# Kernel optimization log

Measured on AMD Instinct MI355X. Metric: run time of the kernel, lower is better.

## Reference

```python
import jax, jax.numpy as jnp
import numpy as np

EPS = 1.1920929e-07  # torch fp32 finfo eps used by F.rms_norm default

def rms_norm(x):
    return x * jax.lax.rsqrt(jnp.mean(jnp.square(x), axis=-1, keepdims=True) + EPS)

def setup_inputs() -> dict:
    key = jax.random.key(0)
    kx, kfc, kpr, krt = jax.random.split(key, 4)
    B, T, C, F = 4, 2048, 2048, 8192
    s = (3.0 ** 0.5) * C ** -0.5  # init scale used in init_weights
    x = jax.random.normal(kx, (B, T, C), dtype=jnp.float32)
    w_fc = jax.random.normal(kfc, (F, C), dtype=jnp.float32) * s
    w_proj = jax.random.normal(kpr, (C, F), dtype=jnp.float32) * (s * 0.1)
    w_router = jax.random.normal(krt, (1, C), dtype=jnp.float32) * 0.01  # router init std=0.01
    return {"x": x, "w_fc": w_fc, "w_proj": w_proj, "w_router": w_router}

def reference(x, w_fc, w_proj, w_router):
    # Router: (B,T,C) @ (C,1) -> (B,T) logits; STE mask (~0 or ~1 floats)
    logits = jnp.einsum('btc,oc->bto', x, w_router)[..., 0]  # (B,T)
    prob = jax.nn.sigmoid(logits)
    hard = (prob > 0.5).astype(x.dtype)
    mask_i = hard + prob - jax.lax.stop_gradient(prob)  # straight-through
    mask_bool = mask_i > 0.5  # (B,T)

    # Gated MLP (mixture-of-depth). The torch code gathers selected tokens,
    # runs the MLP on the compacted set, scatters into zeros, and multiplies
    # by mask_i. Mathematically identical dense form (honoring the mask):
    h = jnp.einsum('btc,fc->btf', rms_norm(x), w_fc)
    h = jnp.square(jax.nn.relu(h))  # relu(x)^2 activation
    mlp_out = jnp.einsum('btf,cf->btc', h, w_proj)
    gated = jnp.where(mask_bool[..., None], mlp_out * mask_i[..., None], 0.0)
    return x + gated
```

## Files before the change

### kernel.cpp

```cpp
#include <hip/hip_runtime.h>
#include <type_traits>
#include <utility>
#include <stdint.h>
#include <stddef.h>

#define TOKENS 8192
#define CDIM 2048
#define FDIM 8192
#define EPSV 1.1920929e-07f

typedef __attribute__((ext_vector_type(8))) short short8;
typedef __attribute__((ext_vector_type(8))) __bf16 bf16x8;
typedef __attribute__((ext_vector_type(4))) float floatx4;

template <typename V, typename = void> struct CanMfma : std::false_type {};
template <typename V>
struct CanMfma<V, std::void_t<decltype(__builtin_amdgcn_mfma_f32_16x16x32_bf16(
    std::declval<V>(), std::declval<V>(), std::declval<floatx4>(), 0, 0, 0))>>
    : std::true_type {};
using frag_t = std::conditional_t<CanMfma<short8>::value, short8, bf16x8>;

__device__ __forceinline__ floatx4 mfma_bf16(frag_t a, frag_t b, floatx4 c) {
    return __builtin_amdgcn_mfma_f32_16x16x32_bf16(a, b, c, 0, 0, 0);
}

__device__ __forceinline__ unsigned short f2bf(float f) {
    unsigned int u = __float_as_uint(f);
    u += 0x7fffu + ((u >> 16) & 1u);
    return (unsigned short)(u >> 16);
}

__global__ void zero_kernel(int* p) { if (threadIdx.x == 0) *p = 0; }

__global__ __launch_bounds__(256) void cvt2_kernel(
    const float* __restrict__ s1, unsigned short* __restrict__ d1, int n1,
    const float* __restrict__ s2, unsigned short* __restrict__ d2, int n2)
{
    int i = blockIdx.x * 256 + threadIdx.x;
    const float4* s; ushort4* d;
    if (i < n1) { s = (const float4*)s1; d = (ushort4*)d1; }
    else if (i < n1 + n2) { s = (const float4*)s2; d = (ushort4*)d2; i -= n1; }
    else return;
    float4 v = s[i];
    ushort4 o;
    o.x = f2bf(v.x); o.y = f2bf(v.y); o.z = f2bf(v.z); o.w = f2bf(v.w);
    d[i] = o;
}

__global__ __launch_bounds__(256) void router_kernel(
    const float* __restrict__ x, const float* __restrict__ wr,
    float* __restrict__ out, unsigned short* __restrict__ Xn,
    int* __restrict__ idx, float* __restrict__ mv, int* __restrict__ cnt)
{
    const int token = blockIdx.x;
    const int tid = threadIdx.x;
    const float4* xr = (const float4*)(x + (size_t)token * CDIM);
    const float4* w4 = (const float4*)wr;
    float4 a0 = xr[tid];
    float4 a1 = xr[tid + 256];
    float4 b0 = w4[tid];
    float4 b1 = w4[tid + 256];
    float ss = a0.x*a0.x + a0.y*a0.y + a0.z*a0.z + a0.w*a0.w
             + a1.x*a1.x + a1.y*a1.y + a1.z*a1.z + a1.w*a1.w;
    float dt = a0.x*b0.x + a0.y*b0.y + a0.z*b0.z + a0.w*b0.w
             + a1.x*b1.x + a1.y*b1.y + a1.z*b1.z + a1.w*b1.w;
    #pragma unroll
    for (int off = 32; off > 0; off >>= 1) {
        ss += __shfl_down(ss, off);
        dt += __shfl_down(dt, off);
    }
    __shared__ float red_ss[4], red_dt[4];
    __shared__ float s_rms;
    __shared__ int s_pos;
    const int wave = tid >> 6;
    if ((tid & 63) == 0) { red_ss[wave] = ss; red_dt[wave] = dt; }
    __syncthreads();
    if (tid == 0) {
        float S = red_ss[0] + red_ss[1] + red_ss[2] + red_ss[3];
        float D = red_dt[0] + red_dt[1] + red_dt[2] + red_dt[3];
        float prob = 1.0f / (1.0f + expf(-D));
        s_rms = 1.0f / sqrtf(S * (1.0f / (float)CDIM) + EPSV);
        int pos = -1;
        if (prob > 0.5f) {
            pos = atomicAdd(cnt, 1);
            idx[pos] = token;
            mv[pos] = (1.0f + prob) - prob;
        }
        s_pos = pos;
    }
    __syncthreads();
    float4* op = (float4*)(out + (size_t)token * CDIM);
    op[tid] = a0;
    op[tid + 256] = a1;
    const float rms = s_rms;
    const int pos = s_pos;
    if (pos >= 0) {
        ushort4* xp = (ushort4*)(Xn + (size_t)pos * CDIM);
        ushort4 o;
        o.x = f2bf(a0.x * rms); o.y = f2bf(a0.y * rms); o.z = f2bf(a0.z * rms); o.w = f2bf(a0.w * rms);
        xp[tid] = o;
        o.x = f2bf(a1.x * rms); o.y = f2bf(a1.y * rms); o.z = f2bf(a1.z * rms); o.w = f2bf(a1.w * rms);
        xp[tid + 256] = o;
    }
}

template <int K, int MODE, int LDO, int KSPLIT>
__global__ __launch_bounds__(256) void gemm_bt(
    const unsigned short* __restrict__ A,
    const unsigned short* __restrict__ B,
    unsigned short* __restrict__ Hout,
    float* __restrict__ out,
    const int* __restrict__ idx,
    const float* __restrict__ mv,
    const int* __restrict__ cntp)
{
    const int cnt = *cntp;
    const int bid = blockIdx.y * 64 + blockIdx.x;
    const int s = bid >> 6;
    const int w = bid & 63;
    const int mi = (s & 7) * 8 + (w & 7);
    const int ni = (s >> 3) * 8 + (w >> 3);
    const int m0 = mi * 128;
    if (m0 >= cnt) return;
    const int n0 = ni * 128;
    const int k0 = (int)blockIdx.z * (K / KSPLIT);

    __shared__ alignas(16) unsigned short lA[128 * 64];
    __shared__ alignas(16) unsigned short lB[128 * 64];

    const int tid = threadIdx.x;
    const int wave = tid >> 6;
    const int lane = tid & 63;
    const int wm = (wave >> 1) * 64;
    const int wn = (wave & 1) * 64;
    const int quad = lane >> 4;
    const int l16 = lane & 15;

    const int srow = lane >> 3;
    const int schunk = (lane & 7) ^ srow;

    const unsigned short* ap[4];
    const unsigned short* bp[4];
    #pragma unroll
    for (int p = 0; p < 4; ++p) {
        const int r = p * 32 + wave * 8 + srow;
        ap[p] = A + (size_t)(m0 + r) * K + k0 + schunk * 8;
        bp[p] = B + (size_t)(n0 + r) * K + k0 + schunk * 8;
    }

    floatx4 acc[4][4] = {};

    for (int kt = 0; kt < K / (64 * KSPLIT); ++kt) {
        #pragma unroll
        for (int p = 0; p < 4; ++p) {
            __builtin_amdgcn_global_load_lds(
                (__attribute__((address_space(1))) void*)ap[p],
                (__attribute__((address_space(3))) void*)&lA[(p * 32 + wave * 8) * 64],
                16, 0, 0);
            __builtin_amdgcn_global_load_lds(
                (__attribute__((address_space(1))) void*)bp[p],
                (__attribute__((address_space(3))) void*)&lB[(p * 32 + wave * 8) * 64],
                16, 0, 0);
            ap[p] += 64;
            bp[p] += 64;
        }
        __syncthreads();
        #pragma unroll
        for (int st = 0; st < 2; ++st) {
            frag_t af[4], bfv[4];
            #pragma unroll
            for (int t = 0; t < 4; ++t) {
                const int ra = wm + t * 16 + l16;
                const int ca = ((st * 4 + quad) ^ (ra & 7)) * 8;
                af[t] = *(const frag_t*)&lA[ra * 64 + ca];
                const int rb = wn + t * 16 + l16;
                const int cb = ((st * 4 + quad) ^ (rb & 7)) * 8;
                bfv[t] = *(const frag_t*)&lB[rb * 64 + cb];
            }
            #pragma unroll
            for (int tm = 0; tm < 4; ++tm)
                #pragma unroll
                for (int tn = 0; tn < 4; ++tn)
                    acc[tm][tn] = mfma_bf16(af[tm], bfv[tn], acc[tm][tn]);
        }
        __syncthreads();
    }

    if (MODE == 1) {
        #pragma unroll
        for (int tm = 0; tm < 4; ++tm) {
            const int gm = m0 + wm + tm * 16 + quad * 4;
            #pragma unroll
            for (int tn = 0; tn < 4; ++tn) {
                const int gn = n0 + wn + tn * 16 + l16;
                #pragma unroll
                for (int v = 0; v < 4; ++v) {
                    float h = fmaxf(acc[tm][tn][v], 0.0f);
                    Hout[(size_t)(gm + v) * LDO + gn] = f2bf(h * h);
                }
            }
        }
    } else {
        #pragma unroll
        for (int tm = 0; tm < 4; ++tm) {
            const int gmb = m0 + wm + tm * 16 + quad * 4;
            #pragma unroll
            for (int v = 0; v < 4; ++v) {
                const int gm = gmb + v;
                if (gm < cnt) {
                    const int token = idx[gm];
                    const float scale = mv[gm];
                    #pragma unroll
                    for (int tn = 0; tn < 4; ++tn) {
                        const int gn = n0 + wn + tn * 16 + l16;
                        atomicAdd(&out[(size_t)token * LDO + gn], scale * acc[tm][tn][v]);
                    }
                }
            }
        }
    }
}

extern "C" void kernel_launch(void* const* d_in, const int* in_sizes, int n_in,
                              void* d_out, int out_size, void* d_ws, size_t ws_size,
                              hipStream_t stream)
{
    const float* x   = (const float*)d_in[0];
    const float* wfc = (const float*)d_in[1];
    const float* wpr = (const float*)d_in[2];
    const float* wrt = (const float*)d_in[3];
    float* out = (float*)d_out;

    char* ws = (char*)d_ws;
    int*   cnt = (int*)ws;
    int*   idx = (int*)(ws + 256);
    float* mv  = (float*)(ws + 256 + 32768);
    unsigned short* Xn  = (unsigned short*)(ws + 65792);
    unsigned short* Wfc = (unsigned short*)(ws + 65792 + 33554432ULL);
    unsigned short* Wpr = (unsigned short*)(ws + 65792 + 67108864ULL);
    unsigned short* H   = (unsigned short*)(ws + 65792 + 100663296ULL);

    const int n4 = FDIM * CDIM / 4;
    zero_kernel<<<1, 64, 0, stream>>>(cnt);
    cvt2_kernel<<<(2 * n4 + 255) / 256, 256, 0, stream>>>(wfc, Wfc, n4, wpr, Wpr, n4);
    router_kernel<<<TOKENS, 256, 0, stream>>>(x, wrt, out, Xn, idx, mv, cnt);
    gemm_bt<CDIM, 1, FDIM, 1><<<dim3(64, FDIM / 128), 256, 0, stream>>>(
        Xn, Wfc, H, nullptr, nullptr, nullptr, cnt);
    gemm_bt<FDIM, 2, CDIM, 2><<<dim3(64, CDIM / 128, 2), 256, 0, stream>>>(
        H, Wpr, nullptr, out, idx, mv, cnt);
}
```

Measured before the change: 704.5 us.

## Double-buffer LDS tiles in GEMM and remap block-to-tile swizzle

Adds a second LDS buffer for the A and B tiles. The next K-slice is issued with global_load_lds before computing on the current one, so global-to-LDS transfer overlaps MFMA work and one barrier per iteration is removed. It also changes the block-to-(m,n) tile mapping within each 64-block group to a 4x... sub-grouping, aiming for better L2 reuse across concurrently running blocks. LDS use doubles to 64KB per block, which may reduce occupancy. Correctness relies on the asynchronous LDS writes being complete at the trailing barrier.

```diff
diff --git a/kernel.cpp b/kernel.cpp
--- a/kernel.cpp
+++ b/kernel.cpp
@@ -118,15 +118,17 @@
     const int bid = blockIdx.y * 64 + blockIdx.x;
     const int s = bid >> 6;
     const int w = bid & 63;
-    const int mi = (s & 7) * 8 + (w & 7);
-    const int ni = (s >> 3) * 8 + (w >> 3);
+    const int r = w & 7;
+    const int t = w >> 3;
+    const int mi = (s & 7) * 8 + (r >> 2) * 4 + (t & 3);
+    const int ni = (s >> 3) * 8 + (r & 3) * 2 + (t >> 2);
     const int m0 = mi * 128;
     if (m0 >= cnt) return;
     const int n0 = ni * 128;
     const int k0 = (int)blockIdx.z * (K / KSPLIT);
 
-    __shared__ alignas(16) unsigned short lA[128 * 64];
-    __shared__ alignas(16) unsigned short lB[128 * 64];
+    __shared__ alignas(16) unsigned short lA[2][128 * 64];
+    __shared__ alignas(16) unsigned short lB[2][128 * 64];
 
     const int tid = threadIdx.x;
     const int wave = tid >> 6;
@@ -143,39 +145,47 @@
     const unsigned short* bp[4];
     #pragma unroll
     for (int p = 0; p < 4; ++p) {
-        const int r = p * 32 + wave * 8 + srow;
-        ap[p] = A + (size_t)(m0 + r) * K + k0 + schunk * 8;
-        bp[p] = B + (size_t)(n0 + r) * K + k0 + schunk * 8;
-    }
-
-    floatx4 acc[4][4] = {};
-
-    for (int kt = 0; kt < K / (64 * KSPLIT); ++kt) {
+        const int rr = p * 32 + wave * 8 + srow;
+        ap[p] = A + (size_t)(m0 + rr) * K + k0 + schunk * 8;
+        bp[p] = B + (size_t)(n0 + rr) * K + k0 + schunk * 8;
+    }
+
+    auto stage = [&](int buf) {
         #pragma unroll
         for (int p = 0; p < 4; ++p) {
             __builtin_amdgcn_global_load_lds(
                 (__attribute__((address_space(1))) void*)ap[p],
-                (__attribute__((address_space(3))) void*)&lA[(p * 32 + wave * 8) * 64],
+                (__attribute__((address_space(3))) void*)&lA[buf][(p * 32 + wave * 8) * 64],
                 16, 0, 0);
             __builtin_amdgcn_global_load_lds(
                 (__attribute__((address_space(1))) void*)bp[p],
-                (__attribute__((address_space(3))) void*)&lB[(p * 32 + wave * 8) * 64],
+                (__attribute__((address_space(3))) void*)&lB[buf][(p * 32 + wave * 8) * 64],
                 16, 0, 0);
             ap[p] += 64;
             bp[p] += 64;
         }
-        __syncthreads();
+    };
+
+    floatx4 acc[4][4] = {};
+
+    const int NT = K / (64 * KSPLIT);
+    int cur = 0;
+    stage(0);
+    __syncthreads();
+
+    for (int kt = 0; kt < NT; ++kt) {
+        if (kt + 1 < NT) stage(cur ^ 1);
         #pragma unroll
         for (int st = 0; st < 2; ++st) {
             frag_t af[4], bfv[4];
             #pragma unroll
-            for (int t = 0; t < 4; ++t) {
-                const int ra = wm + t * 16 + l16;
+            for (int tt = 0; tt < 4; ++tt) {
+                const int ra = wm + tt * 16 + l16;
                 const int ca = ((st * 4 + quad) ^ (ra & 7)) * 8;
-                af[t] = *(const frag_t*)&lA[ra * 64 + ca];
-                const int rb = wn + t * 16 + l16;
+                af[tt] = *(const frag_t*)&lA[cur][ra * 64 + ca];
+                const int rb = wn + tt * 16 + l16;
                 const int cb = ((st * 4 + quad) ^ (rb & 7)) * 8;
-                bfv[t] = *(const frag_t*)&lB[rb * 64 + cb];
+                bfv[tt] = *(const frag_t*)&lB[cur][rb * 64 + cb];
             }
             #pragma unroll
             for (int tm = 0; tm < 4; ++tm)
@@ -184,6 +194,7 @@
                     acc[tm][tn] = mfma_bf16(af[tm], bfv[tn], acc[tm][tn]);
         }
         __syncthreads();
+        cur ^= 1;
     }
 
     if (MODE == 1) {
```

Result: slower. 754.5 us (+7.1%).

## Use 256x256 GEMM tiles with 512 threads and 4-stage LDS pipeline

Applied to the files above, without the earlier changes.

Both bf16 GEMMs now use 256x256 output tiles computed by 8 waves, each wave holding an 8x4 block of MFMA accumulators. The K step drops to 32, and a 4-buffer, 128KB dynamic LDS ring is filled through global_load_lds with three stages in flight. Explicit vmcnt waits, barriers and setprio are added around the MFMA block. The aim is more data reuse per tile and loads that overlap compute, at the cost of higher register pressure, a single block per CU, and fewer blocks for the second GEMM.

```diff
diff --git a/kernel.cpp b/kernel.cpp
--- a/kernel.cpp
+++ b/kernel.cpp
@@ -105,7 +105,7 @@
 }
 
 template <int K, int MODE, int LDO, int KSPLIT>
-__global__ __launch_bounds__(256) void gemm_bt(
+__global__ __launch_bounds__(512, 2) void gemm_bt(
     const unsigned short* __restrict__ A,
     const unsigned short* __restrict__ B,
     unsigned short* __restrict__ Hout,
@@ -115,95 +115,121 @@
     const int* __restrict__ cntp)
 {
     const int cnt = *cntp;
-    const int bid = blockIdx.y * 64 + blockIdx.x;
+    const int bid = blockIdx.y * 32 + blockIdx.x;
     const int s = bid >> 6;
     const int w = bid & 63;
-    const int mi = (s & 7) * 8 + (w & 7);
-    const int ni = (s >> 3) * 8 + (w >> 3);
-    const int m0 = mi * 128;
+    const int mi = (s & 3) * 8 + (w & 7);
+    const int ni = (s >> 2) * 8 + (w >> 3);
+    const int m0 = mi * 256;
     if (m0 >= cnt) return;
-    const int n0 = ni * 128;
+    const int n0 = ni * 256;
     const int k0 = (int)blockIdx.z * (K / KSPLIT);
 
-    __shared__ alignas(16) unsigned short lA[128 * 64];
-    __shared__ alignas(16) unsigned short lB[128 * 64];
+    extern __shared__ unsigned short lds[];
 
     const int tid = threadIdx.x;
     const int wave = tid >> 6;
     const int lane = tid & 63;
-    const int wm = (wave >> 1) * 64;
-    const int wn = (wave & 1) * 64;
+    const int wm = (wave >> 2) * 128;
+    const int wn = (wave & 3) * 64;
     const int quad = lane >> 4;
     const int l16 = lane & 15;
 
-    const int srow = lane >> 3;
-    const int schunk = (lane & 7) ^ srow;
-
-    const unsigned short* ap[4];
-    const unsigned short* bp[4];
+    const int srow = 2 * (tid >> 3) + ((tid >> 2) & 1);
+    const int sq   = (tid & 3) ^ ((tid >> 3) & 3);
+
+    const unsigned short* ap[2];
+    const unsigned short* bp[2];
     #pragma unroll
-    for (int p = 0; p < 4; ++p) {
-        const int r = p * 32 + wave * 8 + srow;
-        ap[p] = A + (size_t)(m0 + r) * K + k0 + schunk * 8;
-        bp[p] = B + (size_t)(n0 + r) * K + k0 + schunk * 8;
-    }
-
-    floatx4 acc[4][4] = {};
-
-    for (int kt = 0; kt < K / (64 * KSPLIT); ++kt) {
-        #pragma unroll
-        for (int p = 0; p < 4; ++p) {
+    for (int p = 0; p < 2; ++p) {
+        const int r = p * 128 + srow;
+        ap[p] = A + (size_t)(m0 + r) * K + k0 + sq * 8;
+        bp[p] = B + (size_t)(n0 + r) * K + k0 + sq * 8;
+    }
+
+    auto stage = [&](int v) {
+        unsigned short* base = &lds[(v & 3) * 16384];
+        #pragma unroll
+        for (int p = 0; p < 2; ++p) {
             __builtin_amdgcn_global_load_lds(
                 (__attribute__((address_space(1))) void*)ap[p],
-                (__attribute__((address_space(3))) void*)&lA[(p * 32 + wave * 8) * 64],
+                (__attribute__((address_space(3))) void*)&base[(p * 512 + wave * 64) * 8],
                 16, 0, 0);
+            ap[p] += 32;
+        }
+        #pragma unroll
+        for (int p = 0; p < 2; ++p) {
             __builtin_amdgcn_global_load_lds(
                 (__attribute__((address_space(1))) void*)bp[p],
-                (__attribute__((address_space(3))) void*)&lB[(p * 32 + wave * 8) * 64],
+                (__attribute__((address_space(3))) void*)&base[8192 + (p * 512 + wave * 64) * 8],
                 16, 0, 0);
-            ap[p] += 64;
-            bp[p] += 64;
-        }
-        __syncthreads();
-        #pragma unroll
-        for (int st = 0; st < 2; ++st) {
-            frag_t af[4], bfv[4];
+            bp[p] += 32;
+        }
+    };
+
+    floatx4 acc[8][4] = {};
+
+    const int NT = K / (32 * KSPLIT);
+    stage(0); stage(1); stage(2);
+
+    for (int u = 0; u < NT; ++u) {
+        const int rem = NT - 1 - u;
+        if (rem >= 3) {
+            stage(u + 3);
+            asm volatile("s_waitcnt vmcnt(12)" ::: "memory");
+        } else if (rem == 2) {
+            asm volatile("s_waitcnt vmcnt(8)" ::: "memory");
+        } else if (rem == 1) {
+            asm volatile("s_waitcnt vmcnt(4)" ::: "memory");
+        } else {
+            asm volatile("s_waitcnt vmcnt(0)" ::: "memory");
+        }
+        __builtin_amdgcn_sched_barrier(0);
+        __builtin_amdgcn_s_barrier();
+        __builtin_amdgcn_sched_barrier(0);
+
+        const unsigned short* sbase = &lds[(u & 3) * 16384];
+        frag_t af[8], bfv[4];
+        #pragma unroll
+        for (int m = 0; m < 8; ++m) {
+            const int ra = wm + m * 16 + l16;
+            af[m] = *(const frag_t*)&sbase[ra * 32 + ((quad ^ ((ra >> 1) & 3)) << 3)];
+        }
+        #pragma unroll
+        for (int n = 0; n < 4; ++n) {
+            const int rb = wn + n * 16 + l16;
+            bfv[n] = *(const frag_t*)&sbase[8192 + rb * 32 + ((quad ^ ((rb >> 1) & 3)) << 3)];
+        }
+        __builtin_amdgcn_s_setprio(1);
+        #pragma unroll
+        for (int m = 0; m < 8; ++m)
             #pragma unroll
-            for (int t = 0; t < 4; ++t) {
-                const int ra = wm + t * 16 + l16;
-                const int ca = ((st * 4 + quad) ^ (ra & 7)) * 8;
-                af[t] = *(const frag_t*)&lA[ra * 64 + ca];
-                const int rb = wn + t * 16 + l16;
-                const int cb = ((st * 4 + quad) ^ (rb & 7)) * 8;
-                bfv[t] = *(const frag_t*)&lB[rb * 64 + cb];
-            }
+            for (int n = 0; n < 4; ++n)
+                acc[m][n] = mfma_bf16(af[m], bfv[n], acc[m][n]);
+        __builtin_amdgcn_s_setprio(0);
+        __builtin_amdgcn_sched_barrier(0);
+        __builtin_amdgcn_s_barrier();
+        __builtin_amdgcn_sched_barrier(0);
+    }
+
+    if (MODE == 1) {
+        #pragma unroll
+        for (int m = 0; m < 8; ++m) {
+            const int gm = m0 + wm + m * 16 + quad * 4;
             #pragma unroll
-            for (int tm = 0; tm < 4; ++tm)
-                #pragma unroll
-                for (int tn = 0; tn < 4; ++tn)
-                    acc[tm][tn] = mfma_bf16(af[tm], bfv[tn], acc[tm][tn]);
-        }
-        __syncthreads();
-    }
-
-    if (MODE == 1) {
-        #pragma unroll
-        for (int tm = 0; tm < 4; ++tm) {
-            const int gm = m0 + wm + tm * 16 + quad * 4;
-            #pragma unroll
-            for (int tn = 0; tn < 4; ++tn) {
-                const int gn = n0 + wn + tn * 16 + l16;
+            for (int n = 0; n < 4; ++n) {
+                const int gn = n0 + wn + n * 16 + l16;
                 #pragma unroll
                 for (int v = 0; v < 4; ++v) {
-                    float h = fmaxf(acc[tm][tn][v], 0.0f);
+                    float h = fmaxf(acc[m][n][v], 0.0f);
                     Hout[(size_t)(gm + v) * LDO + gn] = f2bf(h * h);
                 }
             }
         }
     } else {
         #pragma unroll
-        for (int tm = 0; tm < 4; ++tm) {
-            const int gmb = m0 + wm + tm * 16 + quad * 4;
+        for (int m = 0; m < 8; ++m) {
+            const int gmb = m0 + wm + m * 16 + quad * 4;
             #pragma unroll
             for (int v = 0; v < 4; ++v) {
                 const int gm = gmb + v;
@@ -211,9 +237,9 @@
                     const int token = idx[gm];
                     const float scale = mv[gm];
                     #pragma unroll
-                    for (int tn = 0; tn < 4; ++tn) {
-                        const int gn = n0 + wn + tn * 16 + l16;
-                        atomicAdd(&out[(size_t)token * LDO + gn], scale * acc[tm][tn][v]);
+                    for (int n = 0; n < 4; ++n) {
+                        const int gn = n0 + wn + n * 16 + l16;
+                        atomicAdd(&out[(size_t)token * LDO + gn], scale * acc[m][n][v]);
                     }
                 }
             }
@@ -244,8 +270,8 @@
     zero_kernel<<<1, 64, 0, stream>>>(cnt);
     cvt2_kernel<<<(2 * n4 + 255) / 256, 256, 0, stream>>>(wfc, Wfc, n4, wpr, Wpr, n4);
     router_kernel<<<TOKENS, 256, 0, stream>>>(x, wrt, out, Xn, idx, mv, cnt);
-    gemm_bt<CDIM, 1, FDIM, 1><<<dim3(64, FDIM / 128), 256, 0, stream>>>(
+    gemm_bt<CDIM, 1, FDIM, 1><<<dim3(32, FDIM / 256), 512, 131072, stream>>>(
         Xn, Wfc, H, nullptr, nullptr, nullptr, cnt);
-    gemm_bt<FDIM, 2, CDIM, 2><<<dim3(64, CDIM / 128, 2), 256, 0, stream>>>(
+    gemm_bt<FDIM, 2, CDIM, 2><<<dim3(32, CDIM / 256, 2), 512, 131072, stream>>>(
         H, Wpr, nullptr, out, idx, mv, cnt);
 }
```

Result: no change. 716.2 us (+1.7%).

## Drop split-K atomics in down-projection and write residual directly for routed tokens

Applied to the files above, without the earlier changes.

The second GEMM no longer splits K across two blocks with atomicAdd into a pre-filled output. Each routed token's output is now written once as x plus the scaled MLP result, and the router kernel only copies x to the output for unrouted tokens. Several stores (bf16 weight conversion, normalized activations, H, output) become nontemporal packed stores. Removing split-K halves the grid of the down-projection GEMM, which may reduce parallelism, and the MODE-2 epilogue adds an extra read of x.

```diff
diff --git a/kernel.cpp b/kernel.cpp
--- a/kernel.cpp
+++ b/kernel.cpp
@@ -12,6 +12,8 @@
 typedef __attribute__((ext_vector_type(8))) short short8;
 typedef __attribute__((ext_vector_type(8))) __bf16 bf16x8;
 typedef __attribute__((ext_vector_type(4))) float floatx4;
+typedef __attribute__((ext_vector_type(4))) float f32x4;
+typedef __attribute__((ext_vector_type(2))) unsigned int u32x2;
 
 template <typename V, typename = void> struct CanMfma : std::false_type {};
 template <typename V>
@@ -42,9 +44,10 @@
     else if (i < n1 + n2) { s = (const float4*)s2; d = (ushort4*)d2; i -= n1; }
     else return;
     float4 v = s[i];
-    ushort4 o;
-    o.x = f2bf(v.x); o.y = f2bf(v.y); o.z = f2bf(v.z); o.w = f2bf(v.w);
-    d[i] = o;
+    u32x2 w;
+    w.x = (unsigned)f2bf(v.x) | ((unsigned)f2bf(v.y) << 16);
+    w.y = (unsigned)f2bf(v.z) | ((unsigned)f2bf(v.w) << 16);
+    __builtin_nontemporal_store(w, (u32x2*)&d[i]);
 }
 
 __global__ __launch_bounds__(256) void router_kernel(
@@ -89,18 +92,23 @@
         s_pos = pos;
     }
     __syncthreads();
-    float4* op = (float4*)(out + (size_t)token * CDIM);
-    op[tid] = a0;
-    op[tid + 256] = a1;
     const float rms = s_rms;
     const int pos = s_pos;
-    if (pos >= 0) {
-        ushort4* xp = (ushort4*)(Xn + (size_t)pos * CDIM);
-        ushort4 o;
-        o.x = f2bf(a0.x * rms); o.y = f2bf(a0.y * rms); o.z = f2bf(a0.z * rms); o.w = f2bf(a0.w * rms);
-        xp[tid] = o;
-        o.x = f2bf(a1.x * rms); o.y = f2bf(a1.y * rms); o.z = f2bf(a1.z * rms); o.w = f2bf(a1.w * rms);
-        xp[tid + 256] = o;
+    float* op = out + (size_t)token * CDIM;
+    if (pos < 0) {
+        f32x4 r0 = {a0.x, a0.y, a0.z, a0.w};
+        f32x4 r1 = {a1.x, a1.y, a1.z, a1.w};
+        __builtin_nontemporal_store(r0, (f32x4*)(op + tid * 4));
+        __builtin_nontemporal_store(r1, (f32x4*)(op + (tid + 256) * 4));
+    } else {
+        unsigned short* xp = Xn + (size_t)pos * CDIM;
+        u32x2 w;
+        w.x = (unsigned)f2bf(a0.x * rms) | ((unsigned)f2bf(a0.y * rms) << 16);
+        w.y = (unsigned)f2bf(a0.z * rms) | ((unsigned)f2bf(a0.w * rms) << 16);
+        __builtin_nontemporal_store(w, (u32x2*)(xp + tid * 4));
+        w.x = (unsigned)f2bf(a1.x * rms) | ((unsigned)f2bf(a1.y * rms) << 16);
+        w.y = (unsigned)f2bf(a1.z * rms) | ((unsigned)f2bf(a1.w * rms) << 16);
+        __builtin_nontemporal_store(w, (u32x2*)(xp + (tid + 256) * 4));
     }
 }
 
@@ -110,6 +118,7 @@
     const unsigned short* __restrict__ B,
     unsigned short* __restrict__ Hout,
     float* __restrict__ out,
+    const float* __restrict__ xin,
     const int* __restrict__ idx,
     const float* __restrict__ mv,
     const int* __restrict__ cntp)
@@ -196,7 +205,8 @@
                 #pragma unroll
                 for (int v = 0; v < 4; ++v) {
                     float h = fmaxf(acc[tm][tn][v], 0.0f);
-                    Hout[(size_t)(gm + v) * LDO + gn] = f2bf(h * h);
+                    unsigned short hb = f2bf(h * h);
+                    __builtin_nontemporal_store(hb, &Hout[(size_t)(gm + v) * LDO + gn]);
                 }
             }
         }
@@ -210,10 +220,13 @@
                 if (gm < cnt) {
                     const int token = idx[gm];
                     const float scale = mv[gm];
+                    const float* xrow = xin + (size_t)token * LDO;
+                    float* orow = out + (size_t)token * LDO;
                     #pragma unroll
                     for (int tn = 0; tn < 4; ++tn) {
                         const int gn = n0 + wn + tn * 16 + l16;
-                        atomicAdd(&out[(size_t)token * LDO + gn], scale * acc[tm][tn][v]);
+                        float r = xrow[gn] + scale * acc[tm][tn][v];
+                        __builtin_nontemporal_store(r, &orow[gn]);
                     }
                 }
             }
@@ -245,7 +258,7 @@
     cvt2_kernel<<<(2 * n4 + 255) / 256, 256, 0, stream>>>(wfc, Wfc, n4, wpr, Wpr, n4);
     router_kernel<<<TOKENS, 256, 0, stream>>>(x, wrt, out, Xn, idx, mv, cnt);
     gemm_bt<CDIM, 1, FDIM, 1><<<dim3(64, FDIM / 128), 256, 0, stream>>>(
-        Xn, Wfc, H, nullptr, nullptr, nullptr, cnt);
-    gemm_bt<FDIM, 2, CDIM, 2><<<dim3(64, CDIM / 128, 2), 256, 0, stream>>>(
-        H, Wpr, nullptr, out, idx, mv, cnt);
-}
+        Xn, Wfc, H, nullptr, nullptr, nullptr, nullptr, cnt);
+    gemm_bt<FDIM, 2, CDIM, 1><<<dim3(64, CDIM / 128), 256, 0, stream>>>(
+        H, Wpr, nullptr, out, x, idx, mv, cnt);
+}
```

Measured after the change: 761.6 us. +8.1%, slower.
